# Kernel optimization log

Hardware: AMD Instinct MI355X
Metric: run time of the kernel (lower is better)

The kernel has to match this reference:

```python
import jax, jax.numpy as jnp
from jax import lax
import numpy as np

DN = ('NCDHW', 'OIDHW', 'NCDHW')
ACTIVE_THRESH = 1


def setup_inputs() -> dict:
    key = jax.random.key(0)
    ks = jax.random.split(key, 10)
    B, D = 4, 64
    chans = [3, 64, 128, 256, 512]
    inp = {
        'x': jax.random.normal(ks[0], (B, 3, D, D, D), jnp.float32),
        'mask': jax.random.randint(ks[1], (B, D, D, D), 0, 20, jnp.int32),
    }
    for i in range(4):
        cin, cout = chans[i], chans[i + 1]
        fan_in = cin * 27
        scale = 1.0 / np.sqrt(fan_in)
        inp[f'w{i+1}'] = jax.random.normal(ks[2 + 2 * i], (cout, cin, 3, 3, 3), jnp.float32) * scale
        inp[f'b{i+1}'] = jax.random.normal(ks[3 + 2 * i], (cout,), jnp.float32) * scale
    return inp


def _sparse_block(x, m, w, b, stride):
    # SparseConv3d(k=3, pad=1) + SparseReLU: output active where 3^3 footprint hits an active input;
    # bias + relu applied only at active sites, inactive sites stay exactly 0 (spconv .dense() semantics).
    s = (stride,) * 3
    pad = [(1, 1)] * 3
    y = lax.conv_general_dilated(x, w, s, pad, dimension_numbers=DN)
    ones = jnp.ones((1, 1, 3, 3, 3), x.dtype)
    m_out = lax.conv_general_dilated(m[:, None].astype(x.dtype), ones, s, pad, dimension_numbers=DN) > 0
    y = jnp.where(m_out, jax.nn.relu(y + b[None, :, None, None, None]), jnp.zeros((), x.dtype))
    return y, m_out[:, 0]


def reference(x, mask, w1, b1, w2, b2, w3, b3, w4, b4):
    m = mask < ACTIVE_THRESH                       # [B,D,H,W] active voxels
    h = x * m[:, None].astype(x.dtype)             # zero inactive input features
    h, m = _sparse_block(h, m, w1, b1, 1)          # [B,64,64,64,64]
    h, m = _sparse_block(h, m, w2, b2, 2)          # [B,128,32,32,32]
    h, m = _sparse_block(h, m, w3, b3, 2)          # [B,256,16,16,16]
    h, m = _sparse_block(h, m, w4, b4, 2)          # [B,512,8,8,8]
    pooled = jnp.max(h, axis=(2, 3, 4))            # dense() + amax over D,H,W -> [B,512]
    return jax.nn.leaky_relu(pooled, negative_slope=0.2)
```

## Files before the change

kernel.cpp:

```cpp
#include <hip/hip_runtime.h>

typedef _Float16 f16;
typedef _Float16 half4 __attribute__((ext_vector_type(4)));
typedef _Float16 half8 __attribute__((ext_vector_type(8)));
typedef float f32x4 __attribute__((ext_vector_type(4)));

#define BATCH 4

__device__ __forceinline__ void gload16(const void* g, void* l) {
  __builtin_amdgcn_global_load_lds((const __attribute__((address_space(1))) unsigned int*)g,
                                   (__attribute__((address_space(3))) unsigned int*)l, 16, 0, 0);
}

template<int DP, int ROWB>
__device__ __forceinline__ void zb_one(char* __restrict__ buf, int v, int b) {
  int w = v % DP; int t = v / DP; int h = t % DP; int d = t / DP;
  bool border = (w == 0) | (w == DP - 1) | (h == 0) | (h == DP - 1) | (d == 0) | (d == DP - 1);
  if (!border) return;
  char* p = buf + ((size_t)b * DP * DP * DP + v) * ROWB;
  #pragma unroll
  for (int i = 0; i < ROWB; i += 8)
    *reinterpret_cast<unsigned long long*>(p + i) = 0ull;
}

__global__ __launch_bounds__(256) void wprep_all_k(const float* __restrict__ w1,
                                                   const float* __restrict__ w2,
                                                   const float* __restrict__ w3,
                                                   const float* __restrict__ w4,
                                                   f16* __restrict__ wf1,
                                                   f16* __restrict__ wf2,
                                                   f16* __restrict__ wf3,
                                                   f16* __restrict__ wf4) {
  const int T1 = 64 * 128;
  const int T2 = 27 * 128 * 64;
  const int T3 = 27 * 256 * 128;
  const int T4 = 27 * 512 * 256;
  int idx = blockIdx.x * 256 + threadIdx.x;
  if (idx < T1) {
    int q = idx & 127, co = idx >> 7;
    int k = q >> 2, ci = q & 3;
    float v = (ci < 3 && k < 27) ? w1[(co * 3 + ci) * 27 + k] : 0.f;
    wf1[idx] = (f16)v;
    return;
  }
  idx -= T1;
  const float* w; f16* wo; int COUT, CIN;
  if (idx < T2)       { w = w2; wo = wf2; COUT = 128; CIN = 64; }
  else if ((idx -= T2) < T3) { w = w3; wo = wf3; COUT = 256; CIN = 128; }
  else if ((idx -= T3) < T4) { w = w4; wo = wf4; COUT = 512; CIN = 256; }
  else return;
  int k = idx % 27;
  int t = idx / 27;
  int ci = t % CIN;
  int co = t / CIN;
  wo[((size_t)k * COUT + co) * CIN + ci] = (f16)w[idx];
}

__global__ __launch_bounds__(256) void prep_all_k(const float* __restrict__ x,
                                                  const int* __restrict__ mask,
                                                  f16* __restrict__ xcp,
                                                  char* __restrict__ h1p,
                                                  char* __restrict__ h2p,
                                                  char* __restrict__ h3p) {
  const int D3 = 262144, PD = 66, PD3 = PD * PD * PD;
  const int N3 = 34 * 34 * 34, N4 = 18 * 18 * 18;
  int idx = blockIdx.x * 256 + threadIdx.x;
  int b = blockIdx.y;
  if (idx < PD3) {
    int pv = idx;
    int pw = pv % PD; int t = pv / PD; int ph = t % PD; int pd = t / PD;
    half4 o = {};
    if (pw > 0 && pw < 65 && ph > 0 && ph < 65 && pd > 0 && pd < 65) {
      int v = (((pd - 1) * 64) + (ph - 1)) * 64 + (pw - 1);
      if (mask[(size_t)b * D3 + v] < 1) {
        const float* xb = x + (size_t)b * 3 * D3 + v;
        o[0] = (f16)xb[0];
        o[1] = (f16)xb[D3];
        o[2] = (f16)xb[2 * D3];
      }
    }
    *reinterpret_cast<half4*>(xcp + ((size_t)b * PD3 + pv) * 4) = o;
    return;
  }
  idx -= PD3;
  if (idx < PD3) { zb_one<66, 128>(h1p, idx, b); return; }
  idx -= PD3;
  if (idx < N3) { zb_one<34, 256>(h2p, idx, b); return; }
  idx -= N3;
  if (idx < N4) zb_one<18, 512>(h3p, idx, b);
}

__global__ __launch_bounds__(256) void dil_w_k(const int* __restrict__ mask,
                                               unsigned char* __restrict__ aw) {
  const int D3 = 262144;
  int t = blockIdx.x * 256 + threadIdx.x;
  int b = t >> 16;
  int v = (t & 65535) * 4;
  int w0 = v & 63;
  const int* mb = mask + (size_t)b * D3;
  int a[6];
  a[0] = (w0 > 0) ? (mb[v - 1] < 1) : 0;
  #pragma unroll
  for (int i = 0; i < 4; i++) a[i + 1] = mb[v + i] < 1;
  a[5] = (w0 < 60) ? (mb[v + 4] < 1) : 0;
  unsigned int o = 0;
  #pragma unroll
  for (int i = 0; i < 4; i++)
    o |= ((unsigned)(a[i] | a[i + 1] | a[i + 2])) << (8 * i);
  *reinterpret_cast<unsigned int*>(aw + (size_t)b * D3 + v) = o;
}

__global__ __launch_bounds__(256) void dil_hd2_k(const unsigned char* __restrict__ aw,
                                                 unsigned char* __restrict__ m1) {
  const int D3 = 262144;
  int t = blockIdx.x * 256 + threadIdx.x;
  int b = t >> 16;
  int v = (t & 65535) * 4;
  int h = (v >> 6) & 63;
  int d = v >> 12;
  const unsigned char* ib = aw + (size_t)b * D3;
  unsigned int m = 0;
  #pragma unroll
  for (int dd = -1; dd <= 1; dd++) {
    int id = d + dd; if ((unsigned)id >= 64u) continue;
    #pragma unroll
    for (int hh = -1; hh <= 1; hh++) {
      int ih = h + hh; if ((unsigned)ih >= 64u) continue;
      m |= *reinterpret_cast<const unsigned int*>(ib + ((id << 12) | (ih << 6) | (v & 63)));
    }
  }
  *reinterpret_cast<unsigned int*>(m1 + (size_t)b * D3 + v) = m;
}

__global__ __launch_bounds__(256) void dil_rest_k(const unsigned char* __restrict__ m1,
                                                  unsigned char* __restrict__ m2,
                                                  unsigned char* __restrict__ m3,
                                                  unsigned char* __restrict__ m4,
                                                  float* __restrict__ outp) {
  const int D = 64, D3 = 262144;
  const int S2 = BATCH * 32768, S3 = BATCH * 4096, S4 = BATCH * 512;
  int idx = blockIdx.x * 256 + threadIdx.x;
  int b, v, LOGD, H, ST;
  unsigned char* mo;
  if (idx < S2)                 { b = idx >> 15; v = idx & 32767; LOGD = 5; H = 1; ST = 2; mo = m2 + (size_t)b * 32768; }
  else if ((idx -= S2) < S3)    { b = idx >> 12; v = idx & 4095;  LOGD = 4; H = 3; ST = 4; mo = m3 + (size_t)b * 4096; }
  else if ((idx -= S3) < S4)    { b = idx >> 9;  v = idx & 511;   LOGD = 3; H = 7; ST = 8; mo = m4 + (size_t)b * 512; }
  else if ((idx -= S4) < 2048)  { outp[idx] = 0.f; return; }
  else return;
  int DM = (1 << LOGD) - 1;
  int ow = v & DM, oh = (v >> LOGD) & DM, od = v >> (2 * LOGD);
  const unsigned char* mb = m1 + (size_t)b * D3;
  int act = 0;
  for (int dd = -H; dd <= H && !act; dd++) {
    int id = od * ST + dd; if ((unsigned)id >= (unsigned)D) continue;
    for (int hh = -H; hh <= H && !act; hh++) {
      int ih = oh * ST + hh; if ((unsigned)ih >= (unsigned)D) continue;
      for (int ww = -H; ww <= H; ww++) {
        int iw = ow * ST + ww; if ((unsigned)iw >= (unsigned)D) continue;
        if (mb[((size_t)id * D + ih) * D + iw]) { act = 1; break; }
      }
    }
  }
  mo[v] = (unsigned char)act;
}

template<int BM>
__global__ __launch_bounds__(256) void conv1_mfma_k(const f16* __restrict__ xcp,
                                                    const f16* __restrict__ w1f,
                                                    const float* __restrict__ bias,
                                                    const unsigned char* __restrict__ mo,
                                                    f16* __restrict__ out ) {
  const int D3 = 262144, COUT = 64, PD = 66, PD3 = PD * PD * PD;
  constexpr int K = 128, LDB = K + 8;
  constexpr int WM = 2, WN = 2;
  constexpr int MF = BM / (16 * WM), NF = 64 / (16 * WN);
  __shared__ __align__(16) f16 halo[1056 * 4];
  __shared__ __align__(16) f16 Bs[64][LDB];

  const int tid = threadIdx.x, lane = tid & 63, wave = tid >> 6;
  const int wm = wave >> 1, wn = wave & 1;
  const int v0 = blockIdx.x * BM;
  const int b = blockIdx.y;
  const int oh0 = (v0 >> 6) & 63, od = v0 >> 12;
  const f16* xb = xcp + (size_t)b * PD3 * 4;

  for (int c = tid; c < 64 * (K / 8); c += 256) {
    int row = c >> 4, cc = c & 15;
    *reinterpret_cast<half8*>(&Bs[row][cc * 8]) =
        *reinterpret_cast<const half8*>(w1f + row * K + cc * 8);
  }
  for (int e = tid; e < 1056; e += 256) {
    half4 val = {};
    if (e < 792) {
      int d = e / 264, r = e - d * 264, h = r / 66, w = r - h * 66;
      val = *reinterpret_cast<const half4*>(
          xb + (((size_t)(od + d) * PD + (oh0 + h)) * PD + w) * 4);
    }
    *reinterpret_cast<half4*>(&halo[(size_t)e * 4]) = val;
  }
  __syncthreads();

  const int ll = lane & 15, lh = lane >> 4;
  int koff[8];
  #pragma unroll
  for (int i = 0; i < 8; i++) {
    int ks = (i >> 1) * 8 + 2 * lh + (i & 1);
    int kd = ks / 9, rr = ks - kd * 9, kh = rr / 3, kw = rr - kh * 3;
    koff[i] = ((kd * 4 + kh) * 66 + kw) * 4;
  }
  const int lbase = (wm * 66 + ll) * 4;

  f32x4 acc[MF][NF] = {};
  #pragma unroll
  for (int q = 0; q < 4; q++) {
    half8 a[MF], bb[NF];
    #pragma unroll
    for (int mf = 0; mf < MF; mf++) {
      half4 lo = *reinterpret_cast<const half4*>(&halo[lbase + mf * 64 + koff[q * 2]]);
      half4 hi = *reinterpret_cast<const half4*>(&halo[lbase + mf * 64 + koff[q * 2 + 1]]);
      a[mf] = half8{lo[0], lo[1], lo[2], lo[3], hi[0], hi[1], hi[2], hi[3]};
    }
    #pragma unroll
    for (int nf = 0; nf < NF; nf++)
      bb[nf] = *reinterpret_cast<const half8*>(&Bs[wn * NF * 16 + nf * 16 + ll][q * 32 + lh * 8]);
    #pragma unroll
    for (int mf = 0; mf < MF; mf++)
      #pragma unroll
      for (int nf = 0; nf < NF; nf++)
        acc[mf][nf] = __builtin_amdgcn_mfma_f32_16x16x32_f16(a[mf], bb[nf], acc[mf][nf], 0, 0, 0);
  }

  const unsigned char* mb = mo + (size_t)b * D3;
  f16* ob = out + (size_t)b * PD3 * COUT;
  float bv[NF];
  #pragma unroll
  for (int nf = 0; nf < NF; nf++) bv[nf] = bias[wn * NF * 16 + nf * 16 + ll];
  #pragma unroll
  for (int mf = 0; mf < MF; mf++) {
    #pragma unroll
    for (int r = 0; r < 4; r++) {
      int v = v0 + wm * MF * 16 + mf * 16 + (lh << 2) + r;
      bool act = mb[v] != 0;
      int ow = v & 63, oh = (v >> 6) & 63, odv = v >> 12;
      size_t pv = ((size_t)(odv + 1) * PD + oh + 1) * PD + ow + 1;
      #pragma unroll
      for (int nf = 0; nf < NF; nf++) {
        int co = wn * NF * 16 + nf * 16 + ll;
        float val = acc[mf][nf][r] + bv[nf];
        val = act ? (val > 0.f ? val : 0.f) : 0.f;
        ob[pv * COUT + co] = (f16)val;
      }
    }
  }
}

template<int CINS, int CINF, int COUT, int DIN, int DOUT, int BM, int BN,
         int WM, int WN, int SWZ, int OP, int BMERGE, int POOL>
__global__ __launch_bounds__(WM * WN * 64) void conv_mfma2_k(const f16* __restrict__ in,
                                                             const f16* __restrict__ w27,
                                                             const float* __restrict__ bias,
                                                             const unsigned char* __restrict__ mo,
                                                             f16* __restrict__ out,
                                                             float* __restrict__ poolp) {
  constexpr int PD = DIN + 2, PDo = DOUT + 2;
  constexpr int NW = WM * WN;
  constexpr int MF = BM / (16 * WM), NF = BN / (16 * WN);
  constexpr int ROWB = CINS * 2;
  constexpr int ROWBF = CINF * 2;
  constexpr int CHUNKS = ROWB / 16;
  constexpr int RPI = 64 / CHUNKS;
  constexpr int A_IW = BM / RPI / NW;
  constexpr int B_IW = BN / RPI / NW;
  constexpr int CIH = CINF / CINS;
  constexpr int NSTEP = 27 * CIH;
  constexpr int CI0S = CINS / 32;
  constexpr int D3o = DOUT * DOUT * DOUT;
  constexpr int LOGD = (DOUT == 32) ? 5 : ((DOUT == 16) ? 4 : 3);

  __shared__ __align__(16) char As[2][BM * ROWB];
  __shared__ __align__(16) char Bs[2][BN * ROWB];

  const int tid = threadIdx.x, lane = tid & 63, wave = tid >> 6;
  const int wm = wave / WN, wn = wave % WN;
  int bx = blockIdx.x;
  if (SWZ) {
    int cpx = gridDim.x >> 3;
    bx = (bx & 7) * cpx + (bx >> 3);
  }
  const int v0 = bx * BM, co0 = blockIdx.y * BN;
  const int bz = BMERGE ? 0 : blockIdx.z;

  auto key = [](int r) -> int { return (CHUNKS >= 8) ? (r & 7) : ((r >> 1) & 3); };

  const int lrow = lane / CHUNKS;
  const int lchunk = lane % CHUNKS;
  const char* a_src[A_IW];
  #pragma unroll
  for (int i = 0; i < A_IW; i++) {
    int r = (wave * A_IW + i) * RPI + lrow;
    int v = v0 + r;
    int vb = BMERGE ? (v >> (3 * LOGD)) : bz;
    int vv = BMERGE ? (v & (D3o - 1)) : v;
    int ow = vv & (DOUT - 1), oh = (vv >> LOGD) & (DOUT - 1), od = vv >> (2 * LOGD);
    size_t flat = (size_t)vb * PD * PD * PD + ((size_t)(2 * od) * PD + 2 * oh) * PD + 2 * ow;
    a_src[i] = (const char*)in + flat * ROWBF + (lchunk ^ key(r)) * 16;
  }
  const char* b_src[B_IW];
  #pragma unroll
  for (int i = 0; i < B_IW; i++) {
    int r = (wave * B_IW + i) * RPI + lrow;
    b_src[i] = (const char*)w27 + (size_t)(co0 + r) * ROWBF + (lchunk ^ key(r)) * 16;
  }

  auto stage = [&](int buf, int s) {
    int k = s / CIH;
    int h = s - k * CIH;
    int kd = k / 9, r2 = k - kd * 9, kh = r2 / 3, kw = r2 - kh * 3;
    int koff = ((kd * PD + kh) * PD + kw) * ROWBF + h * ROWB;
    #pragma unroll
    for (int i = 0; i < A_IW; i++)
      gload16(a_src[i] + koff, &As[buf][(wave * A_IW + i) * 1024]);
    size_t wko = (size_t)k * COUT * ROWBF + h * ROWB;
    #pragma unroll
    for (int i = 0; i < B_IW; i++)
      gload16(b_src[i] + wko, &Bs[buf][(wave * B_IW + i) * 1024]);
  };

  f32x4 acc[MF][NF] = {};
  const int ll = lane & 15, lh = lane >> 4;
  const int ra0 = wm * MF * 16 + ll;
  const int rb0 = wn * NF * 16 + ll;
  const int rswa = key(ra0);
  const int rswb = key(rb0);

  stage(0, 0);
  __syncthreads();
  int cur = 0;
  for (int s = 0; s < NSTEP; s++) {
    if (s < NSTEP - 1) stage(cur ^ 1, s + 1);
    #pragma unroll
    for (int c = 0; c < CI0S; c++) {
      const int q = c * 4 + lh;
      half8 a[MF], bb[NF];
      #pragma unroll
      for (int mf = 0; mf < MF; mf++)
        a[mf] = *reinterpret_cast<const half8*>(
            &As[cur][(ra0 + mf * 16) * ROWB + ((q ^ rswa) * 16)]);
      #pragma unroll
      for (int nf = 0; nf < NF; nf++)
        bb[nf] = *reinterpret_cast<const half8*>(
            &Bs[cur][(rb0 + nf * 16) * ROWB + ((q ^ rswb) * 16)]);
      #pragma unroll
      for (int mf = 0; mf < MF; mf++)
        #pragma unroll
        for (int nf = 0; nf < NF; nf++)
          acc[mf][nf] = __builtin_amdgcn_mfma_f32_16x16x32_f16(a[mf], bb[nf], acc[mf][nf], 0, 0, 0);
    }
    __syncthreads();
    cur ^= 1;
  }

  f16* ob = out;
  float bv[NF];
  #pragma unroll
  for (int nf = 0; nf < NF; nf++) bv[nf] = bias[co0 + wn * NF * 16 + nf * 16 + ll];
  float pmax[NF];
  #pragma unroll
  for (int nf = 0; nf < NF; nf++) pmax[nf] = 0.f;
  #pragma unroll
  for (int mf = 0; mf < MF; mf++) {
    #pragma unroll
    for (int r = 0; r < 4; r++) {
      int v = v0 + wm * MF * 16 + mf * 16 + (lh << 2) + r;
      int vb = BMERGE ? (v >> (3 * LOGD)) : bz;
      int vv = BMERGE ? (v & (D3o - 1)) : v;
      bool act = mo[(size_t)vb * D3o + vv] != 0;
      int ow = vv & (DOUT - 1), oh = (vv >> LOGD) & (DOUT - 1), od = vv >> (2 * LOGD);
      size_t pv = OP ? (((size_t)(od + 1) * PDo + oh + 1) * PDo + ow + 1) : (size_t)vv;
      size_t obase = ((size_t)vb * (OP ? PDo * PDo * PDo : D3o) + pv) * COUT;
      #pragma unroll
      for (int nf = 0; nf < NF; nf++) {
        int co = co0 + wn * NF * 16 + nf * 16 + ll;
        float val = acc[mf][nf][r] + bv[nf];
        val = act ? (val > 0.f ? val : 0.f) : 0.f;
        if constexpr (POOL) {
          pmax[nf] = fmaxf(pmax[nf], val);
        } else {
          ob[obase + co] = (f16)val;
        }
      }
    }
  }
  if constexpr (POOL) {
    #pragma unroll
    for (int nf = 0; nf < NF; nf++) {
      int co = co0 + wn * NF * 16 + nf * 16 + ll;
      atomicMax((int*)poolp + bz * 512 + co, __float_as_int(pmax[nf]));
    }
  }
}

extern "C" void kernel_launch(void* const* d_in, const int* in_sizes, int n_in,
                              void* d_out, int out_size, void* d_ws, size_t ws_size,
                              hipStream_t stream) {
  const float* x    = (const float*)d_in[0];
  const int*   mask = (const int*)d_in[1];
  const float* w1 = (const float*)d_in[2];
  const float* b1 = (const float*)d_in[3];
  const float* w2 = (const float*)d_in[4];
  const float* b2 = (const float*)d_in[5];
  const float* w3 = (const float*)d_in[6];
  const float* b3 = (const float*)d_in[7];
  const float* w4 = (const float*)d_in[8];
  const float* b4 = (const float*)d_in[9];
  float* outp = (float*)d_out;

  const size_t PD1 = 66 * 66 * 66;
  const size_t PD2 = 34 * 34 * 34;
  const size_t PD3s = 18 * 18 * 18;

  char* ws = (char*)d_ws;
  size_t off = 0;
  auto alloc = [&](size_t bytes) -> char* {
    char* p = ws + off;
    off = (off + bytes + 255) & ~(size_t)255;
    return p;
  };
  f16* wf1 = (f16*)alloc((size_t)64 * 128 * 2);
  f16* wf2 = (f16*)alloc((size_t)27 * 128 * 64 * 2);
  f16* wf3 = (f16*)alloc((size_t)27 * 256 * 128 * 2);
  f16* wf4 = (f16*)alloc((size_t)27 * 512 * 256 * 2);
  unsigned char* aw = (unsigned char*)alloc((size_t)BATCH * 262144);
  unsigned char* m1 = (unsigned char*)alloc((size_t)BATCH * 262144);
  unsigned char* m2 = (unsigned char*)alloc((size_t)BATCH * 32768);
  unsigned char* m3 = (unsigned char*)alloc((size_t)BATCH * 4096);
  unsigned char* m4 = (unsigned char*)alloc((size_t)BATCH * 512);
  f16* h1p = (f16*)alloc((size_t)BATCH * PD1 * 64 * 2);
  f16* h2p = (f16*)alloc((size_t)BATCH * PD2 * 128 * 2);
  f16* h3p = (f16*)alloc((size_t)BATCH * PD3s * 256 * 2);
  f16* xcp = (f16*)alloc((size_t)BATCH * PD1 * 4 * 2);
  if (off > ws_size) return;

  {
    const int TOT = 64 * 128 + 27 * 128 * 64 + 27 * 256 * 128 + 27 * 512 * 256;
    wprep_all_k<<<dim3((TOT + 255) / 256), 256, 0, stream>>>(w1, w2, w3, w4, wf1, wf2, wf3, wf4);
  }

  dil_w_k<<<dim3(BATCH * 65536 / 256), 256, 0, stream>>>(mask, aw);
  dil_hd2_k<<<dim3(BATCH * 65536 / 256), 256, 0, stream>>>(aw, m1);
  {
    const int TOT = BATCH * 32768 + BATCH * 4096 + BATCH * 512 + 2048;
    dil_rest_k<<<dim3((TOT + 255) / 256), 256, 0, stream>>>(m1, m2, m3, m4, outp);
  }

  {
    const int TOT = 287496 * 2 + 39304 + 5832;
    prep_all_k<<<dim3((TOT + 255) / 256, BATCH), 256, 0, stream>>>(
        x, mask, xcp, (char*)h1p, (char*)h2p, (char*)h3p);
  }

  conv1_mfma_k<128><<<dim3(262144 / 128, BATCH), 256, 0, stream>>>(xcp, wf1, b1, m1, h1p);

  conv_mfma2_k<64, 64, 128, 64, 32, 64, 128, 2, 2, 1, 1, 0, 0>
      <<<dim3(512, 1, BATCH), 256, 0, stream>>>(h1p, wf2, b2, m2, h2p, nullptr);
  conv_mfma2_k<64, 128, 256, 32, 16, 64, 128, 2, 2, 1, 1, 1, 0>
      <<<dim3(256, 2, 1), 256, 0, stream>>>(h2p, wf3, b3, m3, h3p, nullptr);
  conv_mfma2_k<128, 256, 512, 16, 8, 32, 64, 1, 2, 0, 0, 0, 1>
      <<<dim3(16, 8, BATCH), 128, 0, stream>>>(h3p, wf4, b4, m4, nullptr, outp);
}
```

Baseline: 293.2 us.

## Add triple-buffered async-LDS conv kernel for layer 2

```diff
diff --git a/kernel.cpp b/kernel.cpp
--- a/kernel.cpp
+++ b/kernel.cpp
@@ -10,6 +10,12 @@
 __device__ __forceinline__ void gload16(const void* g, void* l) {
   __builtin_amdgcn_global_load_lds((const __attribute__((address_space(1))) unsigned int*)g,
                                    (__attribute__((address_space(3))) unsigned int*)l, 16, 0, 0);
+}
+
+template<int N> __device__ __forceinline__ void wait_vmcnt() {
+  static_assert(N == 0 || N == 6, "add literal");
+  if constexpr (N == 0)      asm volatile("s_waitcnt vmcnt(0)" ::: "memory");
+  else if constexpr (N == 6) asm volatile("s_waitcnt vmcnt(6)" ::: "memory");
 }
 
 template<int DP, int ROWB>
@@ -254,6 +260,132 @@
   }
 }
 
+template<int CIN, int COUT, int DIN, int DOUT, int BM, int BN, int WM, int WN, int SWZ>
+__global__ __launch_bounds__(WM * WN * 64) void conv_p3_k(const f16* __restrict__ in,
+                                                          const f16* __restrict__ w27,
+                                                          const float* __restrict__ bias,
+                                                          const unsigned char* __restrict__ mo,
+                                                          f16* __restrict__ out) {
+  constexpr int PD = DIN + 2, PDo = DOUT + 2;
+  constexpr int NW = WM * WN;
+  constexpr int MF = BM / (16 * WM), NF = BN / (16 * WN);
+  constexpr int ROWB = CIN * 2;
+  constexpr int CHUNKS = ROWB / 16;
+  constexpr int RPI = 64 / CHUNKS;
+  constexpr int A_IW = BM / RPI / NW;
+  constexpr int B_IW = BN / RPI / NW;
+  constexpr int L = A_IW + B_IW;
+  constexpr int CI0S = CIN / 32;
+  constexpr int D3o = DOUT * DOUT * DOUT;
+  constexpr int LOGD = 5;
+
+  __shared__ __align__(16) char As[3][BM * ROWB];
+  __shared__ __align__(16) char Bs[3][BN * ROWB];
+
+  const int tid = threadIdx.x, lane = tid & 63, wave = tid >> 6;
+  const int wm = wave / WN, wn = wave % WN;
+  int bx = blockIdx.x;
+  if (SWZ) {
+    int cpx = gridDim.x >> 3;
+    bx = (bx & 7) * cpx + (bx >> 3);
+  }
+  const int v0 = bx * BM, co0 = blockIdx.y * BN, bz = blockIdx.z;
+
+  const int lrow = lane / CHUNKS;
+  const int lchunk = lane % CHUNKS;
+  const char* a_src[A_IW];
+  #pragma unroll
+  for (int i = 0; i < A_IW; i++) {
+    int r = (wave * A_IW + i) * RPI + lrow;
+    int v = v0 + r;
+    int ow = v & (DOUT - 1), oh = (v >> LOGD) & (DOUT - 1), od = v >> (2 * LOGD);
+    size_t flat = (size_t)bz * PD * PD * PD + ((size_t)(2 * od) * PD + 2 * oh) * PD + 2 * ow;
+    a_src[i] = (const char*)in + flat * ROWB + (lchunk ^ (r & 7)) * 16;
+  }
+  const char* b_src[B_IW];
+  #pragma unroll
+  for (int i = 0; i < B_IW; i++) {
+    int r = (wave * B_IW + i) * RPI + lrow;
+    b_src[i] = (const char*)w27 + (size_t)(co0 + r) * ROWB + (lchunk ^ (r & 7)) * 16;
+  }
+
+  auto stage = [&](int buf, int k) {
+    int kd = k / 9, r2 = k - kd * 9, kh = r2 / 3, kw = r2 - kh * 3;
+    int koff = ((kd * PD + kh) * PD + kw) * ROWB;
+    #pragma unroll
+    for (int i = 0; i < A_IW; i++)
+      gload16(a_src[i] + koff, &As[buf][(wave * A_IW + i) * 1024]);
+    size_t wko = (size_t)k * COUT * ROWB;
+    #pragma unroll
+    for (int i = 0; i < B_IW; i++)
+      gload16(b_src[i] + wko, &Bs[buf][(wave * B_IW + i) * 1024]);
+  };
+
+  f32x4 acc[MF][NF] = {};
+  const int ll = lane & 15, lh = lane >> 4;
+  const int ra0 = wm * MF * 16 + ll;
+  const int rb0 = wn * NF * 16 + ll;
+  const int rswa = ra0 & 7;
+  const int rswb = rb0 & 7;
+
+  stage(0, 0);
+  stage(1, 1);
+  int cur = 0;
+  for (int s = 0; s < 27; s++) {
+    if (s < 26) wait_vmcnt<6>();
+    else        wait_vmcnt<0>();
+    __builtin_amdgcn_s_barrier();
+    asm volatile("" ::: "memory");
+    if (s + 2 < 27) {
+      int nb = cur + 2; if (nb >= 3) nb -= 3;
+      stage(nb, s + 2);
+    }
+    #pragma unroll
+    for (int c = 0; c < CI0S; c++) {
+      const int q = c * 4 + lh;
+      half8 a[MF], bb[NF];
+      #pragma unroll
+      for (int mf = 0; mf < MF; mf++)
+        a[mf] = *reinterpret_cast<const half8*>(
+            &As[cur][(ra0 + mf * 16) * ROWB + ((q ^ rswa) * 16)]);
+      #pragma unroll
+      for (int nf = 0; nf < NF; nf++)
+        bb[nf] = *reinterpret_cast<const half8*>(
+            &Bs[cur][(rb0 + nf * 16) * ROWB + ((q ^ rswb) * 16)]);
+      #pragma unroll
+      for (int mf = 0; mf < MF; mf++)
+        #pragma unroll
+        for (int nf = 0; nf < NF; nf++)
+          acc[mf][nf] = __builtin_amdgcn_mfma_f32_16x16x32_f16(a[mf], bb[nf], acc[mf][nf], 0, 0, 0);
+    }
+    asm volatile("" ::: "memory");
+    cur = (cur + 1 == 3) ? 0 : cur + 1;
+  }
+
+  f16* ob = out;
+  float bv[NF];
+  #pragma unroll
+  for (int nf = 0; nf < NF; nf++) bv[nf] = bias[co0 + wn * NF * 16 + nf * 16 + ll];
+  #pragma unroll
+  for (int mf = 0; mf < MF; mf++) {
+    #pragma unroll
+    for (int r = 0; r < 4; r++) {
+      int v = v0 + wm * MF * 16 + mf * 16 + (lh << 2) + r;
+      bool act = mo[(size_t)bz * D3o + v] != 0;
+      int ow = v & (DOUT - 1), oh = (v >> LOGD) & (DOUT - 1), od = v >> (2 * LOGD);
+      size_t pv = ((size_t)(od + 1) * PDo + oh + 1) * PDo + ow + 1;
+      size_t obase = ((size_t)bz * PDo * PDo * PDo + pv) * COUT;
+      #pragma unroll
+      for (int nf = 0; nf < NF; nf++) {
+        int co = co0 + wn * NF * 16 + nf * 16 + ll;
+        float val = acc[mf][nf][r] + bv[nf];
+        val = act ? (val > 0.f ? val : 0.f) : 0.f;
+        ob[obase + co] = (f16)val;
+      }
+    }
+  }
+}
+
 template<int CINS, int CINF, int COUT, int DIN, int DOUT, int BM, int BN,
          int WM, int WN, int SWZ, int OP, int BMERGE, int POOL>
 __global__ __launch_bounds__(WM * WN * 64) void conv_mfma2_k(const f16* __restrict__ in,
@@ -461,8 +593,8 @@
 
   conv1_mfma_k<128><<<dim3(262144 / 128, BATCH), 256, 0, stream>>>(xcp, wf1, b1, m1, h1p);
 
-  conv_mfma2_k<64, 64, 128, 64, 32, 64, 128, 2, 2, 1, 1, 0, 0>
-      <<<dim3(512, 1, BATCH), 256, 0, stream>>>(h1p, wf2, b2, m2, h2p, nullptr);
+  conv_p3_k<64, 128, 64, 32, 64, 128, 2, 2, 1>
+      <<<dim3(512, 1, BATCH), 256, 0, stream>>>(h1p, wf2, b2, m2, h2p);
   conv_mfma2_k<64, 128, 256, 32, 16, 64, 128, 2, 2, 1, 1, 1, 0>
       <<<dim3(256, 2, 1), 256, 0, stream>>>(h2p, wf3, b3, m3, h3p, nullptr);
   conv_mfma2_k<128, 256, 512, 16, 8, 32, 64, 1, 2, 0, 0, 0, 1>
```

Measured after the change: 304.1 us. +3.7%, slower.
